# Optimization experiments

Measured on AMD Instinct MI355X. Metric: run time of the kernel, lower is better.

## Reference

```python
import jax, jax.numpy as jnp
import numpy as np

B, L, DIM, H, HD = 2, 2048, 1024, 16, 64


def _rope_tables(L, hd):
    inv_freq = 1.0 / (10000.0 ** (np.arange(0, hd, 2, dtype=np.float32) / hd))
    t = np.arange(L, dtype=np.float32)
    freqs = np.outer(t, inv_freq)                 # [L, hd/2]
    emb = np.concatenate([freqs, freqs], axis=-1)  # [L, hd]
    return jnp.asarray(np.cos(emb)), jnp.asarray(np.sin(emb))


def setup_inputs() -> dict:
    key = jax.random.key(0)
    k1, k2, k3 = jax.random.split(key, 3)
    x = jax.random.normal(k1, (B, L, DIM), dtype=jnp.float32)
    cos, sin = _rope_tables(L, HD)
    w_qkv = jax.random.normal(k2, (DIM, 3 * H * HD), dtype=jnp.float32) * (DIM ** -0.5)
    w_out = jax.random.normal(k3, (H * HD, DIM), dtype=jnp.float32) * ((H * HD) ** -0.5)
    return {"x": x, "cos": cos, "sin": sin, "w_qkv": w_qkv, "w_out": w_out}


def _rotate_half(u):
    u1, u2 = jnp.split(u, 2, axis=-1)
    return jnp.concatenate([-u2, u1], axis=-1)


def _apply_rope(u, cos, sin):
    # u: [B, L, H, hd]; cos/sin: [L, hd]
    c = cos[None, :, None, :]
    s = sin[None, :, None, :]
    return u * c + _rotate_half(u) * s


def reference(x, cos, sin, w_qkv, w_out):
    b, l, _ = x.shape
    qkv = jnp.einsum('bld,de->ble', x, w_qkv).reshape(b, l, 3 * H, HD)
    q, k, v = jnp.split(qkv, 3, axis=2)          # each [B, L, H, hd]
    q = _apply_rope(q, cos, sin)
    k = _apply_rope(k, cos, sin)
    scale = HD ** -0.5                            # SDPA default scale
    scores = jnp.einsum('bqhd,bkhd->bhqk', q, k) * scale
    attn = jax.nn.softmax(scores, axis=-1)
    o = jnp.einsum('bhqk,bkhd->bqhd', attn, v).reshape(b, l, H * HD)
    return jnp.einsum('ble,ed->bld', o, w_out)
```

## Files before the change

kernel.cpp:

```cpp
#include <hip/hip_runtime.h>
#include <hip/hip_bf16.h>

#define BATCH 2
#define SEQ   2048
#define DIM   1024
#define NH    16
#define HD    64
#define K_DIM 1024

typedef __attribute__((ext_vector_type(8))) short short8;
typedef __attribute__((ext_vector_type(4))) short short4v;
typedef __attribute__((ext_vector_type(4))) float f32x4;
typedef unsigned short ushort_t;

__device__ __forceinline__ unsigned short f2b(float x) {
    unsigned int u = __float_as_uint(x);
    u += 0x7FFFu + ((u >> 16) & 1u);
    return (unsigned short)(u >> 16);
}

#define ASYNC_COPY16(gp, lp) \
    __builtin_amdgcn_global_load_lds((const __attribute__((address_space(1))) void*)(gp), \
                                     (__attribute__((address_space(3))) void*)(lp), 16, 0, 0)

__global__ __launch_bounds__(256)
void cast_bf16(const float* __restrict__ src, ushort_t* __restrict__ dst, int n4)
{
    int i = blockIdx.x * 256 + threadIdx.x;
    const int stride = gridDim.x * 256;
    for (; i < n4; i += stride) {
        float4 v = ((const float4*)src)[i];
        short4v o;
        o[0] = (short)f2b(v.x); o[1] = (short)f2b(v.y);
        o[2] = (short)f2b(v.z); o[3] = (short)f2b(v.w);
        ((short4v*)dst)[i] = o;
    }
}

__global__ __launch_bounds__(64)
void cast_transpose(const float* __restrict__ src, ushort_t* __restrict__ dst,
                    int K, int N)
{
    const int n  = blockIdx.x * 64 + threadIdx.x;
    const int k0 = blockIdx.y * 8;
    short8 o;
    #pragma unroll
    for (int j = 0; j < 8; ++j) o[j] = (short)f2b(src[(size_t)(k0 + j) * N + n]);
    *(short8*)(dst + (size_t)n * K + k0) = o;
}

__device__ __forceinline__ void gemm_stage(const ushort_t* __restrict__ Ag,
                                           const ushort_t* __restrict__ Bg,
                                           ushort_t* As, ushort_t* Bs,
                                           int k0, int w, int r0, int c0)
{
    ASYNC_COPY16(Ag + (size_t)r0 * K_DIM + k0 + c0 * 8,        As + w * 512);
    ASYNC_COPY16(Ag + (size_t)(64 + r0) * K_DIM + k0 + c0 * 8, As + w * 512 + 2048);
    ASYNC_COPY16(Bg + (size_t)r0 * K_DIM + k0 + c0 * 8,        Bs + w * 512);
    ASYNC_COPY16(Bg + (size_t)(64 + r0) * K_DIM + k0 + c0 * 8, Bs + w * 512 + 2048);
}

__device__ __forceinline__ void mfma_gemm_tile(
    const ushort_t* __restrict__ Ag, const ushort_t* __restrict__ Bg,
    ushort_t (&As)[2][128 * 32], ushort_t (&Bs)[2][128 * 32], f32x4 acc[4][4])
{
    const int t = threadIdx.x;
    const int w = t >> 6, lane = t & 63;
    const int qd = lane >> 4, cl = lane & 15;
    const int p0 = w * 64 + lane;
    const int r0 = p0 >> 2;
    const int c0 = (p0 & 3) ^ (r0 & 3);

    gemm_stage(Ag, Bg, As[0], Bs[0], 0, w, r0, c0);

    for (int kt = 0; kt < K_DIM / 32; ++kt) {
        const int cur = kt & 1;
        __syncthreads();
        if (kt + 1 < K_DIM / 32)
            gemm_stage(Ag, Bg, As[cur ^ 1], Bs[cur ^ 1], (kt + 1) * 32, w, r0, c0);

        short8 af[4], bfr[4];
        #pragma unroll
        for (int rt = 0; rt < 4; ++rt) {
            const int row = (w >> 1) * 64 + rt * 16 + cl;
            af[rt] = *(const short8*)(As[cur] + row * 32 + ((qd ^ (row & 3)) * 8));
        }
        #pragma unroll
        for (int ct = 0; ct < 4; ++ct) {
            const int col = (w & 1) * 64 + ct * 16 + cl;
            bfr[ct] = *(const short8*)(Bs[cur] + col * 32 + ((qd ^ (col & 3)) * 8));
        }
        #pragma unroll
        for (int rt = 0; rt < 4; ++rt)
            #pragma unroll
            for (int ct = 0; ct < 4; ++ct)
                acc[rt][ct] = __builtin_amdgcn_mfma_f32_16x16x32_bf16(
                    af[rt], bfr[ct], acc[rt][ct], 0, 0, 0);
    }
}

__global__ __launch_bounds__(256, 3)
void gemm_qkv_mfma(const ushort_t* __restrict__ xb, const ushort_t* __restrict__ wqb,
                   ushort_t* __restrict__ qb, ushort_t* __restrict__ kb,
                   ushort_t* __restrict__ vt,
                   const float* __restrict__ cosb, const float* __restrict__ sinb)
{
    __shared__ __align__(16) ushort_t As[2][128 * 32];
    __shared__ __align__(16) ushort_t Bs[2][128 * 32];
    const int m0 = blockIdx.y * 128, n0 = blockIdx.x * 128;

    f32x4 acc[4][4];
    #pragma unroll
    for (int i = 0; i < 4; ++i)
        #pragma unroll
        for (int j = 0; j < 4; ++j)
            #pragma unroll
            for (int r = 0; r < 4; ++r) acc[i][j][r] = 0.f;

    mfma_gemm_tile(xb + (size_t)m0 * K_DIM, wqb + (size_t)n0 * K_DIM, As, Bs, acc);

    const int t = threadIdx.x, w = t >> 6, lane = t & 63;
    const int qd = lane >> 4, cl = lane & 15;
    const int b = m0 >> 11;
    const int lbase = (m0 & 2047) + (w >> 1) * 64;
    const int region = blockIdx.x >> 3;
    const int h = (blockIdx.x & 7) * 2 + (w & 1);

    if (region < 2) {
        ushort_t* dst = region ? kb : qb;
        const float sc = region ? 1.0f : 0.18033688011111234f;
        #pragma unroll
        for (int rt = 0; rt < 4; ++rt) {
            #pragma unroll
            for (int r = 0; r < 4; ++r) {
                const int l = lbase + rt * 16 + qd * 4 + r;
                const float c0 = cosb[l * HD + cl],      s0 = sinb[l * HD + cl];
                const float c1 = cosb[l * HD + 16 + cl], s1 = sinb[l * HD + 16 + cl];
                const float v0 = acc[rt][0][r] * c0 - acc[rt][2][r] * s0;
                const float v1 = acc[rt][1][r] * c1 - acc[rt][3][r] * s1;
                const float v2 = acc[rt][2][r] * c0 + acc[rt][0][r] * s0;
                const float v3 = acc[rt][3][r] * c1 + acc[rt][1][r] * s1;
                ushort_t* p = dst + (((size_t)b * NH + h) * SEQ + l) * HD;
                p[cl]      = f2b(v0 * sc);
                p[16 + cl] = f2b(v1 * sc);
                p[32 + cl] = f2b(v2 * sc);
                p[48 + cl] = f2b(v3 * sc);
            }
        }
    } else {
        #pragma unroll
        for (int rt = 0; rt < 4; ++rt)
            #pragma unroll
            for (int ct = 0; ct < 4; ++ct) {
                const int d = ct * 16 + cl;
                const int l = lbase + rt * 16 + qd * 4;
                short4v o4;
                #pragma unroll
                for (int r = 0; r < 4; ++r) o4[r] = (short)f2b(acc[rt][ct][r]);
                *(short4v*)(vt + (((size_t)b * NH + h) * HD + d) * SEQ + l) = o4;
            }
    }
}

__global__ __launch_bounds__(256, 3)
void gemm_out_mfma(const ushort_t* __restrict__ ob, const ushort_t* __restrict__ wob,
                   float* __restrict__ out)
{
    __shared__ __align__(16) ushort_t As[2][128 * 32];
    __shared__ __align__(16) ushort_t Bs[2][128 * 32];
    const int m0 = blockIdx.y * 128, n0 = blockIdx.x * 128;

    f32x4 acc[4][4];
    #pragma unroll
    for (int i = 0; i < 4; ++i)
        #pragma unroll
        for (int j = 0; j < 4; ++j)
            #pragma unroll
            for (int r = 0; r < 4; ++r) acc[i][j][r] = 0.f;

    mfma_gemm_tile(ob + (size_t)m0 * K_DIM, wob + (size_t)n0 * K_DIM, As, Bs, acc);

    const int t = threadIdx.x, w = t >> 6, lane = t & 63;
    const int qd = lane >> 4, cl = lane & 15;
    const int mbase = m0 + (w >> 1) * 64, nbase = n0 + (w & 1) * 64;
    #pragma unroll
    for (int rt = 0; rt < 4; ++rt)
        #pragma unroll
        for (int ct = 0; ct < 4; ++ct)
            #pragma unroll
            for (int r = 0; r < 4; ++r)
                out[(size_t)(mbase + rt * 16 + qd * 4 + r) * DIM + nbase + ct * 16 + cl] =
                    acc[rt][ct][r];
}

__global__ __launch_bounds__(256, 3)
void attn_mfma(const ushort_t* __restrict__ qb, const ushort_t* __restrict__ kb,
               const ushort_t* __restrict__ vt, float* __restrict__ Op,
               float* __restrict__ lp)
{
    const int h = blockIdx.x;
    const int b = blockIdx.y >> 1;
    const int half = blockIdx.y & 1;
    const int qt = blockIdx.z;
    const int t = threadIdx.x;
    const int w = t >> 6, lane = t & 63;
    const int qd = lane >> 4, cl = lane & 15;
    constexpr int NT = SEQ / 64 / 2;

    __shared__ __align__(16) ushort_t Ks[2][64 * 64];
    __shared__ __align__(16) ushort_t Vs[2][64 * 64];
    __shared__ __align__(16) ushort_t P[4][2048];
    char* Pb = (char*)P[w];

    const size_t bh = (size_t)b * NH + h;
    const ushort_t* qbase = qb + (bh * SEQ + qt * 128 + w * 32) * HD;
    const ushort_t* kbase = kb + bh * SEQ * HD;
    const ushort_t* vbase = vt + bh * (size_t)HD * SEQ;

    const int p0 = w * 128 + lane;
    const int r0a = p0 >> 3,  c0a = (p0 & 7) ^ (r0a & 7);
    const int p1 = p0 + 64;
    const int r1a = p1 >> 3,  c1a = (p1 & 7) ^ (r1a & 7);
    const int ldsoff0 = (w * 128) * 8;
    const int ldsoff1 = (w * 128 + 64) * 8;

    short8 qf[2][2];
    #pragma unroll
    for (int nt = 0; nt < 2; ++nt)
        #pragma unroll
        for (int kh = 0; kh < 2; ++kh)
            qf[nt][kh] = *(const short8*)(qbase + (nt * 16 + cl) * HD + kh * 32 + qd * 8);

    f32x4 oaccT[4][2];
    float l_part[2] = {0.f, 0.f};
    #pragma unroll
    for (int dt = 0; dt < 4; ++dt)
        #pragma unroll
        for (int nt = 0; nt < 2; ++nt)
            #pragma unroll
            for (int r = 0; r < 4; ++r) oaccT[dt][nt][r] = 0.f;

    short8 pf_prev[2][2], vf_prev[4][2];
    #pragma unroll
    for (int nt = 0; nt < 2; ++nt)
        #pragma unroll
        for (int kh = 0; kh < 2; ++kh)
            #pragma unroll
            for (int e = 0; e < 8; ++e) pf_prev[nt][kh][e] = 0;
    #pragma unroll
    for (int dt = 0; dt < 4; ++dt)
        #pragma unroll
        for (int kh = 0; kh < 2; ++kh)
            #pragma unroll
            for (int e = 0; e < 8; ++e) vf_prev[dt][kh][e] = 0;

    const int g0 = half * NT;
    {
        ASYNC_COPY16(kbase + (size_t)(g0 * 64 + r0a) * HD + c0a * 8, (ushort_t*)Ks[0] + ldsoff0);
        ASYNC_COPY16(kbase + (size_t)(g0 * 64 + r1a) * HD + c1a * 8, (ushort_t*)Ks[0] + ldsoff1);
        ASYNC_COPY16(vbase + (size_t)r0a * SEQ + g0 * 64 + c0a * 8,  (ushort_t*)Vs[0] + ldsoff0);
        ASYNC_COPY16(vbase + (size_t)r1a * SEQ + g0 * 64 + c1a * 8,  (ushort_t*)Vs[0] + ldsoff1);
    }

    for (int kt = 0; kt < NT; ++kt) {
        const int cur = kt & 1;
        __syncthreads();
        if (kt + 1 < NT) {
            const int g = g0 + kt + 1;
            ASYNC_COPY16(kbase + (size_t)(g * 64 + r0a) * HD + c0a * 8, (ushort_t*)Ks[cur ^ 1] + ldsoff0);
            ASYNC_COPY16(kbase + (size_t)(g * 64 + r1a) * HD + c1a * 8, (ushort_t*)Ks[cur ^ 1] + ldsoff1);
            ASYNC_COPY16(vbase + (size_t)r0a * SEQ + g * 64 + c0a * 8,  (ushort_t*)Vs[cur ^ 1] + ldsoff0);
            ASYNC_COPY16(vbase + (size_t)r1a * SEQ + g * 64 + c1a * 8,  (ushort_t*)Vs[cur ^ 1] + ldsoff1);
        }

        short8 kf[4][2], vf[4][2];
        #pragma unroll
        for (int mt = 0; mt < 4; ++mt)
            #pragma unroll
            for (int kh = 0; kh < 2; ++kh)
                kf[mt][kh] = *(const short8*)(Ks[cur] + ((mt * 16 + cl) * 8 + ((kh * 4 + qd) ^ (cl & 7))) * 8);
        #pragma unroll
        for (int dt = 0; dt < 4; ++dt)
            #pragma unroll
            for (int kh = 0; kh < 2; ++kh)
                vf[dt][kh] = *(const short8*)(Vs[cur] + ((dt * 16 + cl) * 8 + ((kh * 4 + qd) ^ (cl & 7))) * 8);

        f32x4 s[4][2];
        #pragma unroll
        for (int mt = 0; mt < 4; ++mt)
            #pragma unroll
            for (int nt = 0; nt < 2; ++nt)
                #pragma unroll
                for (int r = 0; r < 4; ++r) s[mt][nt][r] = 0.f;
        #pragma unroll
        for (int kh = 0; kh < 2; ++kh)
            #pragma unroll
            for (int mt = 0; mt < 4; ++mt)
                #pragma unroll
                for (int nt = 0; nt < 2; ++nt)
                    s[mt][nt] = __builtin_amdgcn_mfma_f32_16x16x32_bf16(
                        kf[mt][kh], qf[nt][kh], s[mt][nt], 0, 0, 0);

        #pragma unroll
        for (int kh = 0; kh < 2; ++kh)
            #pragma unroll
            for (int dt = 0; dt < 4; ++dt)
                #pragma unroll
                for (int nt = 0; nt < 2; ++nt)
                    oaccT[dt][nt] = __builtin_amdgcn_mfma_f32_16x16x32_bf16(
                        vf_prev[dt][kh], pf_prev[nt][kh], oaccT[dt][nt], 0, 0, 0);

        #pragma unroll
        for (int nt = 0; nt < 2; ++nt) {
            #pragma unroll
            for (int mt = 0; mt < 4; ++mt) {
                const float e0 = __builtin_amdgcn_exp2f(s[mt][nt][0]);
                const float e1 = __builtin_amdgcn_exp2f(s[mt][nt][1]);
                const float e2 = __builtin_amdgcn_exp2f(s[mt][nt][2]);
                const float e3 = __builtin_amdgcn_exp2f(s[mt][nt][3]);
                l_part[nt] += (e0 + e1) + (e2 + e3);
                union { __hip_bfloat162 h2[2]; unsigned long long u64; } pk;
                pk.h2[0] = __float22bfloat162_rn(make_float2(e0, e1));
                pk.h2[1] = __float22bfloat162_rn(make_float2(e2, e3));
                const int g = (mt * 2 + (qd >> 1)) ^ (cl & 7);
                *(unsigned long long*)(Pb + (nt * 16 + cl) * 128 + g * 16 + (qd & 1) * 8) = pk.u64;
            }
        }
        __builtin_amdgcn_wave_barrier();

        #pragma unroll
        for (int nt = 0; nt < 2; ++nt)
            #pragma unroll
            for (int kh = 0; kh < 2; ++kh)
                pf_prev[nt][kh] = *(const short8*)(Pb + (nt * 16 + cl) * 128 + (((kh * 4 + qd) ^ (cl & 7)) * 16));
        #pragma unroll
        for (int dt = 0; dt < 4; ++dt)
            #pragma unroll
            for (int kh = 0; kh < 2; ++kh)
                vf_prev[dt][kh] = vf[dt][kh];
    }

    #pragma unroll
    for (int kh = 0; kh < 2; ++kh)
        #pragma unroll
        for (int dt = 0; dt < 4; ++dt)
            #pragma unroll
            for (int nt = 0; nt < 2; ++nt)
                oaccT[dt][nt] = __builtin_amdgcn_mfma_f32_16x16x32_bf16(
                    vf_prev[dt][kh], pf_prev[nt][kh], oaccT[dt][nt], 0, 0, 0);

    #pragma unroll
    for (int nt = 0; nt < 2; ++nt) {
        float l = l_part[nt];
        l += __shfl_xor(l, 16);
        l += __shfl_xor(l, 32);
        const int query = qt * 128 + w * 32 + nt * 16 + cl;
        if (qd == 0)
            lp[((size_t)half * BATCH + b) * NH * SEQ + ((size_t)h) * SEQ + query
               + (size_t)b * 0] = l;
        float* op = Op + (((size_t)half * BATCH + b) * SEQ + query) * DIM + h * HD;
        #pragma unroll
        for (int dt = 0; dt < 4; ++dt)
            *(f32x4*)(op + dt * 16 + qd * 4) = oaccT[dt][nt];
    }
}

__global__ __launch_bounds__(256)
void reduce_o(const float* __restrict__ Op, const float* __restrict__ lp,
              ushort_t* __restrict__ ob)
{
    const int idx = blockIdx.x * 256 + threadIdx.x;
    const int d4 = idx & 255;
    const int l  = (idx >> 8) & 2047;
    const int b  = idx >> 19;
    const int h  = d4 >> 4;

    const size_t o_off = ((size_t)b * SEQ + l) * DIM + d4 * 4;
    const float4 a = *(const float4*)(Op + o_off);
    const float4 c = *(const float4*)(Op + (size_t)BATCH * SEQ * DIM + o_off);
    const size_t l_off = ((size_t)b * NH + h) * SEQ + l;
    const float inv = 1.0f / (lp[l_off] + lp[(size_t)BATCH * NH * SEQ + l_off]);

    short4v o4;
    o4[0] = (short)f2b((a.x + c.x) * inv);
    o4[1] = (short)f2b((a.y + c.y) * inv);
    o4[2] = (short)f2b((a.z + c.z) * inv);
    o4[3] = (short)f2b((a.w + c.w) * inv);
    *(short4v*)(ob + o_off) = o4;
}

extern "C" void kernel_launch(void* const* d_in, const int* in_sizes, int n_in,
                              void* d_out, int out_size, void* d_ws, size_t ws_size,
                              hipStream_t stream)
{
    const float* x     = (const float*)d_in[0];
    const float* cosb  = (const float*)d_in[1];
    const float* sinb  = (const float*)d_in[2];
    const float* w_qkv = (const float*)d_in[3];
    const float* w_out = (const float*)d_in[4];
    float* out = (float*)d_out;

    constexpr size_t MB = 1u << 20;
    char* ws = (char*)d_ws;
    ushort_t* qb  = (ushort_t*)(ws);
    ushort_t* kb  = (ushort_t*)(ws + 8 * MB);
    ushort_t* vt  = (ushort_t*)(ws + 16 * MB);
    ushort_t* wob = (ushort_t*)(ws + 24 * MB);
    float*    lp  = (float*)   (ws + 26 * MB);
    float*    Op  = (float*)   (ws + 27 * MB);
    ushort_t* xb  = (ushort_t*)(ws + 27 * MB);
    ushort_t* wqb = (ushort_t*)(ws + 35 * MB);
    ushort_t* ob  = qb;

    constexpr size_t XN = (size_t)BATCH * SEQ * DIM;

    cast_bf16<<<1024, 256, 0, stream>>>(x, xb, (int)(XN / 4));
    cast_transpose<<<dim3(48, 128), 64, 0, stream>>>(w_qkv, wqb, 1024, 3072);
    cast_transpose<<<dim3(16, 128), 64, 0, stream>>>(w_out, wob, 1024, 1024);

    gemm_qkv_mfma<<<dim3(24, 32), 256, 0, stream>>>(xb, wqb, qb, kb, vt, cosb, sinb);
    attn_mfma<<<dim3(16, 4, 16), 256, 0, stream>>>(qb, kb, vt, Op, lp);
    reduce_o<<<4096, 256, 0, stream>>>(Op, lp, ob);
    gemm_out_mfma<<<dim3(8, 32), 256, 0, stream>>>(ob, wob, out);
}
```

Measured before the change: 209.6 us.

## Merge cast kernels into one launch and single-buffer attention K/V tiles

```diff
diff --git a/kernel.cpp b/kernel.cpp
--- a/kernel.cpp
+++ b/kernel.cpp
@@ -24,29 +24,35 @@
                                      (__attribute__((address_space(3))) void*)(lp), 16, 0, 0)
 
 __global__ __launch_bounds__(256)
-void cast_bf16(const float* __restrict__ src, ushort_t* __restrict__ dst, int n4)
-{
-    int i = blockIdx.x * 256 + threadIdx.x;
-    const int stride = gridDim.x * 256;
-    for (; i < n4; i += stride) {
-        float4 v = ((const float4*)src)[i];
-        short4v o;
-        o[0] = (short)f2b(v.x); o[1] = (short)f2b(v.y);
-        o[2] = (short)f2b(v.z); o[3] = (short)f2b(v.w);
-        ((short4v*)dst)[i] = o;
-    }
-}
-
-__global__ __launch_bounds__(64)
-void cast_transpose(const float* __restrict__ src, ushort_t* __restrict__ dst,
-                    int K, int N)
-{
-    const int n  = blockIdx.x * 64 + threadIdx.x;
-    const int k0 = blockIdx.y * 8;
-    short8 o;
-    #pragma unroll
-    for (int j = 0; j < 8; ++j) o[j] = (short)f2b(src[(size_t)(k0 + j) * N + n]);
-    *(short8*)(dst + (size_t)n * K + k0) = o;
+void prep(const float* __restrict__ x, const float* __restrict__ w_qkv,
+          const float* __restrict__ w_out, ushort_t* __restrict__ xb,
+          ushort_t* __restrict__ wqb, ushort_t* __restrict__ wob)
+{
+    const int bid = blockIdx.x;
+    if (bid < 1024) {
+        constexpr int n4 = (BATCH * SEQ * DIM) / 4;
+        int i = bid * 256 + threadIdx.x;
+        for (; i < n4; i += 1024 * 256) {
+            float4 v = ((const float4*)x)[i];
+            short4v o;
+            o[0] = (short)f2b(v.x); o[1] = (short)f2b(v.y);
+            o[2] = (short)f2b(v.z); o[3] = (short)f2b(v.w);
+            ((short4v*)xb)[i] = o;
+        }
+    } else {
+        const int lane = threadIdx.x & 63;
+        const float* src; ushort_t* dst; int N, job;
+        if (bid < 2560) { src = w_qkv; dst = wqb; N = 3072; job = (bid - 1024) * 4 + (threadIdx.x >> 6); }
+        else            { src = w_out; dst = wob; N = 1024; job = (bid - 2560) * 4 + (threadIdx.x >> 6); }
+        const int jn = (N == 3072) ? (job % 48) : (job % 16);
+        const int jk = (N == 3072) ? (job / 48) : (job / 16);
+        const int n  = jn * 64 + lane;
+        const int k0 = jk * 8;
+        short8 o;
+        #pragma unroll
+        for (int j = 0; j < 8; ++j) o[j] = (short)f2b(src[(size_t)(k0 + j) * N + n]);
+        *(short8*)(dst + (size_t)n * K_DIM + k0) = o;
+    }
 }
 
 __device__ __forceinline__ void gemm_stage(const ushort_t* __restrict__ Ag,
@@ -193,7 +199,7 @@
                     acc[rt][ct][r];
 }
 
-__global__ __launch_bounds__(256, 3)
+__global__ __launch_bounds__(256, 4)
 void attn_mfma(const ushort_t* __restrict__ qb, const ushort_t* __restrict__ kb,
                const ushort_t* __restrict__ vt, float* __restrict__ Op,
                float* __restrict__ lp)
@@ -207,8 +213,8 @@
     const int qd = lane >> 4, cl = lane & 15;
     constexpr int NT = SEQ / 64 / 2;
 
-    __shared__ __align__(16) ushort_t Ks[2][64 * 64];
-    __shared__ __align__(16) ushort_t Vs[2][64 * 64];
+    __shared__ __align__(16) ushort_t Ks[64 * 64];
+    __shared__ __align__(16) ushort_t Vs[64 * 64];
     __shared__ __align__(16) ushort_t P[4][2048];
     char* Pb = (char*)P[w];
 
@@ -256,34 +262,36 @@
 
     const int g0 = half * NT;
     {
-        ASYNC_COPY16(kbase + (size_t)(g0 * 64 + r0a) * HD + c0a * 8, (ushort_t*)Ks[0] + ldsoff0);
-        ASYNC_COPY16(kbase + (size_t)(g0 * 64 + r1a) * HD + c1a * 8, (ushort_t*)Ks[0] + ldsoff1);
-        ASYNC_COPY16(vbase + (size_t)r0a * SEQ + g0 * 64 + c0a * 8,  (ushort_t*)Vs[0] + ldsoff0);
-        ASYNC_COPY16(vbase + (size_t)r1a * SEQ + g0 * 64 + c1a * 8,  (ushort_t*)Vs[0] + ldsoff1);
+        ASYNC_COPY16(kbase + (size_t)(g0 * 64 + r0a) * HD + c0a * 8, Ks + ldsoff0);
+        ASYNC_COPY16(kbase + (size_t)(g0 * 64 + r1a) * HD + c1a * 8, Ks + ldsoff1);
+        ASYNC_COPY16(vbase + (size_t)r0a * SEQ + g0 * 64 + c0a * 8,  Vs + ldsoff0);
+        ASYNC_COPY16(vbase + (size_t)r1a * SEQ + g0 * 64 + c1a * 8,  Vs + ldsoff1);
     }
 
     for (int kt = 0; kt < NT; ++kt) {
-        const int cur = kt & 1;
         __syncthreads();
+
+        short8 kf[4][2], vf[4][2];
+        #pragma unroll
+        for (int mt = 0; mt < 4; ++mt)
+            #pragma unroll
+            for (int kh = 0; kh < 2; ++kh)
+                kf[mt][kh] = *(const short8*)(Ks + ((mt * 16 + cl) * 8 + ((kh * 4 + qd) ^ (cl & 7))) * 8);
+        #pragma unroll
+        for (int dt = 0; dt < 4; ++dt)
+            #pragma unroll
+            for (int kh = 0; kh < 2; ++kh)
+                vf[dt][kh] = *(const short8*)(Vs + ((dt * 16 + cl) * 8 + ((kh * 4 + qd) ^ (cl & 7))) * 8);
+
+        __syncthreads();
+
         if (kt + 1 < NT) {
             const int g = g0 + kt + 1;
-            ASYNC_COPY16(kbase + (size_t)(g * 64 + r0a) * HD + c0a * 8, (ushort_t*)Ks[cur ^ 1] + ldsoff0);
-            ASYNC_COPY16(kbase + (size_t)(g * 64 + r1a) * HD + c1a * 8, (ushort_t*)Ks[cur ^ 1] + ldsoff1);
-            ASYNC_COPY16(vbase + (size_t)r0a * SEQ + g * 64 + c0a * 8,  (ushort_t*)Vs[cur ^ 1] + ldsoff0);
-            ASYNC_COPY16(vbase + (size_t)r1a * SEQ + g * 64 + c1a * 8,  (ushort_t*)Vs[cur ^ 1] + ldsoff1);
-        }
-
-        short8 kf[4][2], vf[4][2];
-        #pragma unroll
-        for (int mt = 0; mt < 4; ++mt)
-            #pragma unroll
-            for (int kh = 0; kh < 2; ++kh)
-                kf[mt][kh] = *(const short8*)(Ks[cur] + ((mt * 16 + cl) * 8 + ((kh * 4 + qd) ^ (cl & 7))) * 8);
-        #pragma unroll
-        for (int dt = 0; dt < 4; ++dt)
-            #pragma unroll
-            for (int kh = 0; kh < 2; ++kh)
-                vf[dt][kh] = *(const short8*)(Vs[cur] + ((dt * 16 + cl) * 8 + ((kh * 4 + qd) ^ (cl & 7))) * 8);
+            ASYNC_COPY16(kbase + (size_t)(g * 64 + r0a) * HD + c0a * 8, Ks + ldsoff0);
+            ASYNC_COPY16(kbase + (size_t)(g * 64 + r1a) * HD + c1a * 8, Ks + ldsoff1);
+            ASYNC_COPY16(vbase + (size_t)r0a * SEQ + g * 64 + c0a * 8,  Vs + ldsoff0);
+            ASYNC_COPY16(vbase + (size_t)r1a * SEQ + g * 64 + c1a * 8,  Vs + ldsoff1);
+        }
 
         f32x4 s[4][2];
         #pragma unroll
@@ -356,8 +364,7 @@
         l += __shfl_xor(l, 32);
         const int query = qt * 128 + w * 32 + nt * 16 + cl;
         if (qd == 0)
-            lp[((size_t)half * BATCH + b) * NH * SEQ + ((size_t)h) * SEQ + query
-               + (size_t)b * 0] = l;
+            lp[((size_t)half * BATCH + b) * NH * SEQ + (size_t)h * SEQ + query] = l;
         float* op = Op + (((size_t)half * BATCH + b) * SEQ + query) * DIM + h * HD;
         #pragma unroll
         for (int dt = 0; dt < 4; ++dt)
@@ -412,12 +419,7 @@
     ushort_t* wqb = (ushort_t*)(ws + 35 * MB);
     ushort_t* ob  = qb;
 
-    constexpr size_t XN = (size_t)BATCH * SEQ * DIM;
-
-    cast_bf16<<<1024, 256, 0, stream>>>(x, xb, (int)(XN / 4));
-    cast_transpose<<<dim3(48, 128), 64, 0, stream>>>(w_qkv, wqb, 1024, 3072);
-    cast_transpose<<<dim3(16, 128), 64, 0, stream>>>(w_out, wob, 1024, 1024);
-
+    prep<<<3072, 256, 0, stream>>>(x, w_qkv, w_out, xb, wqb, wob);
     gemm_qkv_mfma<<<dim3(24, 32), 256, 0, stream>>>(xb, wqb, qb, kb, vt, cosb, sinb);
     attn_mfma<<<dim3(16, 4, 16), 256, 0, stream>>>(qb, kb, vt, Op, lp);
     reduce_o<<<4096, 256, 0, stream>>>(Op, lp, ob);
```

Result: slower. 262.9 us (+25.4%).
